# Performance work log

Hardware: AMD Instinct MI355X
Metric: run time of the kernel (lower is better)

## Reference

```python
import jax, jax.numpy as jnp
import numpy as np

L = 16            # number_of_grid_levels
T = 524288        # max_hash_table_entries (2^19)
F = 2             # hash_table_feature_dim
MIN_RES = 16      # coarsest_resolution
MAX_RES = 2048    # finest_resolution
WIDTH = 64        # mlp_width
OUT = 3           # output_channels
N = 1048576       # number of 2D query points
PRIME_Y = np.uint32(2654435761)  # NGP spatial hash prime for dim 1 (dim 0 prime = 1)


def _resolutions():
    g = np.exp((np.log(MAX_RES) - np.log(MIN_RES)) / (L - 1))
    return np.floor(MIN_RES * g ** np.arange(L)).astype(np.float32)  # [L]


def setup_inputs() -> dict:
    key = jax.random.key(0)
    ks = jax.random.split(key, 6)
    x = jax.random.uniform(ks[0], (N, 2), dtype=jnp.float32)
    # NGP hash tables are initialized small uniform
    tables = jax.random.uniform(ks[1], (L, T, F), minval=-1e-4, maxval=1e-4, dtype=jnp.float32)
    def dense(k, fi, fo):
        return (jax.random.normal(k, (fi, fo), dtype=jnp.float32) / np.sqrt(fi).astype(np.float32))
    W0 = dense(ks[2], L * F, WIDTH)
    W1 = dense(ks[3], WIDTH, WIDTH)
    W2 = dense(ks[4], WIDTH, OUT)
    return dict(x=x, tables=tables,
                W0=W0, b0=jnp.zeros((WIDTH,), jnp.float32),
                W1=W1, b1=jnp.zeros((WIDTH,), jnp.float32),
                W2=W2, b2=jnp.zeros((OUT,), jnp.float32))


def _hash_encode(x, tables):
    # Multi-resolution hash grid encoding (Instant-NGP, spatial_dim=2).
    res = jnp.asarray(_resolutions())                  # [L]
    scaled = x[:, None, :] * res[None, :, None]        # [N, L, 2]
    floored = jnp.floor(scaled)
    frac = scaled - floored                            # [N, L, 2]
    corners = jnp.array([[0, 0], [1, 0], [0, 1], [1, 1]], dtype=jnp.int32)  # [4, 2]
    vert = floored.astype(jnp.int32)[:, :, None, :] + corners[None, None]   # [N, L, 4, 2]
    vu = vert.astype(jnp.uint32)
    h = vu[..., 0] ^ (vu[..., 1] * PRIME_Y)            # spatial hash (prime for dim0 is 1)
    idx = (h % jnp.uint32(T)).astype(jnp.int32)        # [N, L, 4]
    feats = tables[jnp.arange(L)[None, :, None], idx]  # [N, L, 4, F] gather per level
    # bilinear weights: prod over dims of frac (if corner==1) else 1-frac
    wd = jnp.where(corners[None, None] == 1, frac[:, :, None, :], 1.0 - frac[:, :, None, :])
    w = wd[..., 0] * wd[..., 1]                        # [N, L, 4]
    interp = jnp.einsum('nlc,nlcf->nlf', w, feats)     # [N, L, F]
    return interp.reshape(x.shape[0], L * F)           # [N, L*F]


def reference(x, tables, W0, b0, W1, b1, W2, b2):
    h = _hash_encode(x, tables)
    h = jax.nn.relu(h @ W0 + b0)
    h = jax.nn.relu(h @ W1 + b1)
    return jax.nn.sigmoid(h @ W2 + b2)   # [N, 3]
```

## Files before the change

kernel.cpp:

```cpp
#include <hip/hip_runtime.h>

#define LVLS  16
#define TSZ   524288u
#define TMASK (TSZ - 1u)
#define PRIME 2654435761u

__constant__ float RES[LVLS] = {16.f, 22.f, 30.f, 42.f, 58.f, 80.f, 111.f, 153.f,
                                212.f, 294.f, 406.f, 561.f, 776.f, 1072.f, 1482.f, 2048.f};

typedef __bf16 bf16x8 __attribute__((ext_vector_type(8)));
typedef float  f32x4  __attribute__((ext_vector_type(4)));

union Frag {
    uint4          q;
    unsigned       u[4];
    unsigned short s[8];
    bf16x8         v;
};

static __device__ __forceinline__ unsigned short f2bf(float f) {
    unsigned u = __float_as_uint(f);
    u += 0x7FFFu + ((u >> 16) & 1u);
    return (unsigned short)(u >> 16);
}
static __device__ __forceinline__ unsigned pack2(float a, float b) {
    return (unsigned)f2bf(a) | ((unsigned)f2bf(b) << 16);
}
static __device__ __forceinline__ void lds_fence() {
    asm volatile("s_waitcnt lgkmcnt(0)" ::: "memory");
}

__global__ __launch_bounds__(256) void ngp_encode(
    const float* __restrict__ x, const float* __restrict__ tables,
    unsigned* __restrict__ feat, int N, int PB)
{
    const int g  = blockIdx.x;
    const int r  = g & 7;
    const int i  = g >> 3;
    const int hi = (i >= PB);
    const int l  = r + (hi << 3);
    const int pb = i - (hi ? PB : 0);
    const int n  = pb * 256 + threadIdx.x;
    if (n >= N) return;

    const float2 xy = ((const float2*)x)[n];
    const float res = RES[l];
    const float sx = xy.x * res, sy = xy.y * res;
    const float fx = floorf(sx),  fy = floorf(sy);
    const float ux = sx - fx,     uy = sy - fy;
    const unsigned ix = (unsigned)(int)fx, iy = (unsigned)(int)fy;
    const unsigned hy0 = iy * PRIME, hy1 = (iy + 1u) * PRIME;
    const unsigned i00 = (ix ^ hy0) & TMASK;
    const unsigned i10 = ((ix + 1u) ^ hy0) & TMASK;
    const unsigned i01 = (ix ^ hy1) & TMASK;
    const unsigned i11 = ((ix + 1u) ^ hy1) & TMASK;
    const float2* tb = (const float2*)(tables + (size_t)l * (TSZ * 2));
    const float2 f00 = tb[i00], f10 = tb[i10], f01 = tb[i01], f11 = tb[i11];
    const float w00 = (1.f - ux) * (1.f - uy);
    const float w10 = ux * (1.f - uy);
    const float w01 = (1.f - ux) * uy;
    const float w11 = ux * uy;
    const float e0 = w00*f00.x + w10*f10.x + w01*f01.x + w11*f11.x;
    const float e1 = w00*f00.y + w10*f10.y + w01*f01.y + w11*f11.y;
    feat[(size_t)l * N + n] = pack2(e0, e1);
}

__global__ __launch_bounds__(256) void ngp_mlp(
    const unsigned* __restrict__ feat,
    const float* __restrict__ W0, const float* __restrict__ b0,
    const float* __restrict__ W1, const float* __restrict__ b1,
    const float* __restrict__ W2, const float* __restrict__ b2,
    float* __restrict__ out, int N)
{
    __shared__ uint4 sB0[4 * 64];
    __shared__ uint4 sB1[8 * 64];
    __shared__ uint4 sB2[2 * 64];
    __shared__ __align__(16) unsigned short hscr[4][16][72];

    const int tid  = threadIdx.x;
    const int lane = tid & 63;
    const int w    = tid >> 6;
    const int c    = lane & 15;
    const int quad = lane >> 4;

    {
        const int f = tid >> 6;
        Frag t0;
        #pragma unroll
        for (int j = 0; j < 8; ++j)
            t0.s[j] = f2bf(W0[(quad * 8 + j) * 64 + f * 16 + c]);
        sB0[f * 64 + lane] = t0.q;

        #pragma unroll
        for (int pass = 0; pass < 2; ++pass) {
            const int ff = f + pass * 4;
            const int kt = ff >> 2, tt = ff & 3;
            Frag t1;
            #pragma unroll
            for (int j = 0; j < 8; ++j)
                t1.s[j] = f2bf(W1[(kt * 32 + quad * 8 + j) * 64 + tt * 16 + c]);
            sB1[ff * 64 + lane] = t1.q;
        }
        if (f < 2) {
            Frag t2;
            #pragma unroll
            for (int j = 0; j < 8; ++j) {
                const float v = (c < 3) ? W2[(f * 32 + quad * 8 + j) * 3 + c] : 0.f;
                t2.s[j] = f2bf(v);
            }
            sB2[f * 64 + lane] = t2.q;
        }
    }
    __syncthreads();

    Frag B0f[4], B1f[8], B2f[2];
    #pragma unroll
    for (int t = 0; t < 4; ++t) B0f[t].q = sB0[t * 64 + lane];
    #pragma unroll
    for (int f = 0; f < 8; ++f) B1f[f].q = sB1[f * 64 + lane];
    #pragma unroll
    for (int f = 0; f < 2; ++f) B2f[f].q = sB2[f * 64 + lane];

    float bias0[4], bias1[4];
    #pragma unroll
    for (int t = 0; t < 4; ++t) { bias0[t] = b0[t * 16 + c]; bias1[t] = b1[t * 16 + c]; }
    const float bias2 = (c < 3) ? b2[c] : 0.f;

    #pragma unroll 1
    for (int it = 0; it < 4; ++it) {
        const int n0 = blockIdx.x * 256 + w * 64 + it * 16;

        Frag a0;
        #pragma unroll
        for (int i = 0; i < 4; ++i)
            a0.u[i] = feat[(size_t)(quad * 4 + i) * N + n0 + c];

        f32x4 acc0[4];
        #pragma unroll
        for (int t = 0; t < 4; ++t) {
            f32x4 cin = {bias0[t], bias0[t], bias0[t], bias0[t]};
            acc0[t] = __builtin_amdgcn_mfma_f32_16x16x32_bf16(a0.v, B0f[t].v, cin, 0, 0, 0);
        }

        lds_fence();
        #pragma unroll
        for (int t = 0; t < 4; ++t)
            #pragma unroll
            for (int rr = 0; rr < 4; ++rr)
                hscr[w][quad * 4 + rr][t * 16 + c] = f2bf(fmaxf(acc0[t][rr], 0.f));

        lds_fence();
        Frag a1[2];
        #pragma unroll
        for (int kt = 0; kt < 2; ++kt)
            a1[kt].q = *(const uint4*)&hscr[w][c][kt * 32 + quad * 8];

        f32x4 acc1[4];
        #pragma unroll
        for (int t = 0; t < 4; ++t) {
            f32x4 cin = {bias1[t], bias1[t], bias1[t], bias1[t]};
            cin = __builtin_amdgcn_mfma_f32_16x16x32_bf16(a1[0].v, B1f[t].v, cin, 0, 0, 0);
            acc1[t] = __builtin_amdgcn_mfma_f32_16x16x32_bf16(a1[1].v, B1f[4 + t].v, cin, 0, 0, 0);
        }

        lds_fence();
        #pragma unroll
        for (int t = 0; t < 4; ++t)
            #pragma unroll
            for (int rr = 0; rr < 4; ++rr)
                hscr[w][quad * 4 + rr][t * 16 + c] = f2bf(fmaxf(acc1[t][rr], 0.f));

        lds_fence();
        Frag a2[2];
        #pragma unroll
        for (int kt = 0; kt < 2; ++kt)
            a2[kt].q = *(const uint4*)&hscr[w][c][kt * 32 + quad * 8];

        f32x4 cin2 = {bias2, bias2, bias2, bias2};
        cin2 = __builtin_amdgcn_mfma_f32_16x16x32_bf16(a2[0].v, B2f[0].v, cin2, 0, 0, 0);
        f32x4 acc2 = __builtin_amdgcn_mfma_f32_16x16x32_bf16(a2[1].v, B2f[1].v, cin2, 0, 0, 0);

        if (c < 3) {
            #pragma unroll
            for (int rr = 0; rr < 4; ++rr) {
                const float s = 1.f / (1.f + __expf(-acc2[rr]));
                out[(size_t)(n0 + quad * 4 + rr) * 3 + c] = s;
            }
        }
    }
}

extern "C" void kernel_launch(void* const* d_in, const int* in_sizes, int n_in,
                              void* d_out, int out_size, void* d_ws, size_t ws_size,
                              hipStream_t stream) {
    const float* x      = (const float*)d_in[0];
    const float* tables = (const float*)d_in[1];
    const float* W0     = (const float*)d_in[2];
    const float* b0     = (const float*)d_in[3];
    const float* W1     = (const float*)d_in[4];
    const float* b1     = (const float*)d_in[5];
    const float* W2     = (const float*)d_in[6];
    const float* b2     = (const float*)d_in[7];
    float* out = (float*)d_out;
    unsigned* feat = (unsigned*)d_ws;

    const int N  = in_sizes[0] / 2;
    const int PB = (N + 255) / 256;
    ngp_encode<<<16 * PB, 256, 0, stream>>>(x, tables, feat, N, PB);
    ngp_mlp<<<PB, 256, 0, stream>>>(feat, W0, b0, W1, b1, W2, b2, out, N);
}
```

Measured before the change: 308.2 us.

## Sort query points into spatial cells before hash encoding for gather locality

Points are bucketed into a 256x256 grid with a histogram, scan and scatter. The encoder then reads them in spatially sorted order, so neighbouring threads hit nearby hash table entries and gathers get better cache locality. The MLP writes its outputs back through the permutation. Weight fragments are precomputed once by a separate kernel instead of in every block, and each wave now processes 128 points with two tiles in flight. The cost is four extra launches plus atomic histogram and scatter passes, and the output stores become scattered.

```diff
diff --git a/kernel.cpp b/kernel.cpp
--- a/kernel.cpp
+++ b/kernel.cpp
@@ -29,9 +29,87 @@
 static __device__ __forceinline__ void lds_fence() {
     asm volatile("s_waitcnt lgkmcnt(0)" ::: "memory");
 }
+static __device__ __forceinline__ unsigned cell_key(float2 v) {
+    unsigned cx = (unsigned)(v.x * 256.f); cx = cx > 255u ? 255u : cx;
+    unsigned cy = (unsigned)(v.y * 256.f); cy = cy > 255u ? 255u : cy;
+    return (cy << 8) | cx;
+}
+
+__global__ __launch_bounds__(256) void k_zero(unsigned* __restrict__ hist) {
+    hist[blockIdx.x * 256 + threadIdx.x] = 0u;
+}
+
+__global__ __launch_bounds__(256) void k_hist(const float2* __restrict__ x,
+                                              unsigned* __restrict__ hist, int N) {
+    const int n = blockIdx.x * 256 + threadIdx.x;
+    if (n >= N) return;
+    atomicAdd(&hist[cell_key(x[n])], 1u);
+}
+
+__global__ __launch_bounds__(1024) void k_scan(unsigned* __restrict__ hist) {
+    __shared__ unsigned ps[1024];
+    const int t = threadIdx.x;
+    unsigned s = 0;
+    for (int i = 0; i < 64; ++i) s += hist[t * 64 + i];
+    ps[t] = s;
+    __syncthreads();
+    for (int off = 1; off < 1024; off <<= 1) {
+        const unsigned v = (t >= off) ? ps[t - off] : 0u;
+        __syncthreads();
+        ps[t] += v;
+        __syncthreads();
+    }
+    unsigned run = ps[t] - s;
+    for (int i = 0; i < 64; ++i) {
+        const unsigned cnt = hist[t * 64 + i];
+        hist[t * 64 + i] = run;
+        run += cnt;
+    }
+}
+
+__global__ __launch_bounds__(256) void k_scatter(const float2* __restrict__ x,
+                                                 unsigned* __restrict__ hist,
+                                                 int* __restrict__ perm,
+                                                 float2* __restrict__ xs, int N) {
+    const int n = blockIdx.x * 256 + threadIdx.x;
+    if (n >= N) return;
+    const float2 v = x[n];
+    const unsigned pos = atomicAdd(&hist[cell_key(v)], 1u);
+    perm[pos] = n;
+    xs[pos] = v;
+}
+
+__global__ __launch_bounds__(64) void k_frag(
+    const float* __restrict__ W0, const float* __restrict__ W1,
+    const float* __restrict__ W2, uint4* __restrict__ frg)
+{
+    const int lane = threadIdx.x;
+    const int c = lane & 15, quad = lane >> 4;
+    Frag t;
+    for (int f = 0; f < 4; ++f) {
+        #pragma unroll
+        for (int j = 0; j < 8; ++j) t.s[j] = f2bf(W0[(quad * 8 + j) * 64 + f * 16 + c]);
+        frg[f * 64 + lane] = t.q;
+    }
+    for (int ff = 0; ff < 8; ++ff) {
+        const int kt = ff >> 2, tt = ff & 3;
+        #pragma unroll
+        for (int j = 0; j < 8; ++j)
+            t.s[j] = f2bf(W1[(kt * 32 + quad * 8 + j) * 64 + tt * 16 + c]);
+        frg[(4 + ff) * 64 + lane] = t.q;
+    }
+    for (int f = 0; f < 2; ++f) {
+        #pragma unroll
+        for (int j = 0; j < 8; ++j) {
+            const float v = (c < 3) ? W2[(f * 32 + quad * 8 + j) * 3 + c] : 0.f;
+            t.s[j] = f2bf(v);
+        }
+        frg[(12 + f) * 64 + lane] = t.q;
+    }
+}
 
 __global__ __launch_bounds__(256) void ngp_encode(
-    const float* __restrict__ x, const float* __restrict__ tables,
+    const float2* __restrict__ xs, const float* __restrict__ tables,
     unsigned* __restrict__ feat, int N, int PB)
 {
     const int g  = blockIdx.x;
@@ -43,7 +121,7 @@
     const int n  = pb * 256 + threadIdx.x;
     if (n >= N) return;
 
-    const float2 xy = ((const float2*)x)[n];
+    const float2 xy = xs[n];
     const float res = RES[l];
     const float sx = xy.x * res, sy = xy.y * res;
     const float fx = floorf(sx),  fy = floorf(sy);
@@ -66,16 +144,12 @@
 }
 
 __global__ __launch_bounds__(256) void ngp_mlp(
-    const unsigned* __restrict__ feat,
-    const float* __restrict__ W0, const float* __restrict__ b0,
-    const float* __restrict__ W1, const float* __restrict__ b1,
-    const float* __restrict__ W2, const float* __restrict__ b2,
-    float* __restrict__ out, int N)
+    const unsigned* __restrict__ feat, const uint4* __restrict__ frg,
+    const float* __restrict__ b0, const float* __restrict__ b1,
+    const float* __restrict__ b2,
+    const int* __restrict__ perm, float* __restrict__ out, int N)
 {
-    __shared__ uint4 sB0[4 * 64];
-    __shared__ uint4 sB1[8 * 64];
-    __shared__ uint4 sB2[2 * 64];
-    __shared__ __align__(16) unsigned short hscr[4][16][72];
+    __shared__ __align__(16) unsigned short hscr[4][2][16][72];
 
     const int tid  = threadIdx.x;
     const int lane = tid & 63;
@@ -83,108 +157,107 @@
     const int c    = lane & 15;
     const int quad = lane >> 4;
 
-    {
-        const int f = tid >> 6;
-        Frag t0;
-        #pragma unroll
-        for (int j = 0; j < 8; ++j)
-            t0.s[j] = f2bf(W0[(quad * 8 + j) * 64 + f * 16 + c]);
-        sB0[f * 64 + lane] = t0.q;
-
-        #pragma unroll
-        for (int pass = 0; pass < 2; ++pass) {
-            const int ff = f + pass * 4;
-            const int kt = ff >> 2, tt = ff & 3;
-            Frag t1;
-            #pragma unroll
-            for (int j = 0; j < 8; ++j)
-                t1.s[j] = f2bf(W1[(kt * 32 + quad * 8 + j) * 64 + tt * 16 + c]);
-            sB1[ff * 64 + lane] = t1.q;
-        }
-        if (f < 2) {
-            Frag t2;
-            #pragma unroll
-            for (int j = 0; j < 8; ++j) {
-                const float v = (c < 3) ? W2[(f * 32 + quad * 8 + j) * 3 + c] : 0.f;
-                t2.s[j] = f2bf(v);
-            }
-            sB2[f * 64 + lane] = t2.q;
-        }
-    }
-    __syncthreads();
-
     Frag B0f[4], B1f[8], B2f[2];
     #pragma unroll
-    for (int t = 0; t < 4; ++t) B0f[t].q = sB0[t * 64 + lane];
-    #pragma unroll
-    for (int f = 0; f < 8; ++f) B1f[f].q = sB1[f * 64 + lane];
-    #pragma unroll
-    for (int f = 0; f < 2; ++f) B2f[f].q = sB2[f * 64 + lane];
+    for (int t = 0; t < 4; ++t) B0f[t].q = frg[t * 64 + lane];
+    #pragma unroll
+    for (int f = 0; f < 8; ++f) B1f[f].q = frg[(4 + f) * 64 + lane];
+    #pragma unroll
+    for (int f = 0; f < 2; ++f) B2f[f].q = frg[(12 + f) * 64 + lane];
 
     float bias0[4], bias1[4];
     #pragma unroll
     for (int t = 0; t < 4; ++t) { bias0[t] = b0[t * 16 + c]; bias1[t] = b1[t * 16 + c]; }
     const float bias2 = (c < 3) ? b2[c] : 0.f;
 
-    #pragma unroll 1
-    for (int it = 0; it < 4; ++it) {
-        const int n0 = blockIdx.x * 256 + w * 64 + it * 16;
-
-        Frag a0;
+    const int base = blockIdx.x * 512 + w * 128;
+
+    Frag a0[8];
+    #pragma unroll
+    for (int tt = 0; tt < 8; ++tt)
         #pragma unroll
         for (int i = 0; i < 4; ++i)
-            a0.u[i] = feat[(size_t)(quad * 4 + i) * N + n0 + c];
-
-        f32x4 acc0[4];
-        #pragma unroll
-        for (int t = 0; t < 4; ++t) {
-            f32x4 cin = {bias0[t], bias0[t], bias0[t], bias0[t]};
-            acc0[t] = __builtin_amdgcn_mfma_f32_16x16x32_bf16(a0.v, B0f[t].v, cin, 0, 0, 0);
-        }
+            a0[tt].u[i] = feat[(size_t)(quad * 4 + i) * N + base + tt * 16 + c];
+
+    #pragma unroll
+    for (int gpair = 0; gpair < 4; ++gpair) {
+        const int t0n = base + (2 * gpair) * 16;
+        const int t1n = base + (2 * gpair + 1) * 16;
+        if (t0n + 16 > N) break;
+
+        int p[2][4];
+        #pragma unroll
+        for (int s = 0; s < 2; ++s)
+            #pragma unroll
+            for (int rr = 0; rr < 4; ++rr) {
+                const int idx = (s ? t1n : t0n) + quad * 4 + rr;
+                p[s][rr] = perm ? perm[idx] : idx;
+            }
+
+        f32x4 acc[2][4];
+        #pragma unroll
+        for (int s = 0; s < 2; ++s)
+            #pragma unroll
+            for (int t = 0; t < 4; ++t) {
+                f32x4 cin = {bias0[t], bias0[t], bias0[t], bias0[t]};
+                acc[s][t] = __builtin_amdgcn_mfma_f32_16x16x32_bf16(
+                    a0[2 * gpair + s].v, B0f[t].v, cin, 0, 0, 0);
+            }
 
         lds_fence();
         #pragma unroll
-        for (int t = 0; t < 4; ++t)
-            #pragma unroll
-            for (int rr = 0; rr < 4; ++rr)
-                hscr[w][quad * 4 + rr][t * 16 + c] = f2bf(fmaxf(acc0[t][rr], 0.f));
-
+        for (int s = 0; s < 2; ++s)
+            #pragma unroll
+            for (int t = 0; t < 4; ++t)
+                #pragma unroll
+                for (int rr = 0; rr < 4; ++rr)
+                    hscr[w][s][quad * 4 + rr][t * 16 + c] = f2bf(fmaxf(acc[s][t][rr], 0.f));
         lds_fence();
-        Frag a1[2];
-        #pragma unroll
-        for (int kt = 0; kt < 2; ++kt)
-            a1[kt].q = *(const uint4*)&hscr[w][c][kt * 32 + quad * 8];
-
-        f32x4 acc1[4];
-        #pragma unroll
-        for (int t = 0; t < 4; ++t) {
-            f32x4 cin = {bias1[t], bias1[t], bias1[t], bias1[t]};
-            cin = __builtin_amdgcn_mfma_f32_16x16x32_bf16(a1[0].v, B1f[t].v, cin, 0, 0, 0);
-            acc1[t] = __builtin_amdgcn_mfma_f32_16x16x32_bf16(a1[1].v, B1f[4 + t].v, cin, 0, 0, 0);
-        }
+
+        Frag a1[2][2];
+        #pragma unroll
+        for (int s = 0; s < 2; ++s)
+            #pragma unroll
+            for (int kt = 0; kt < 2; ++kt)
+                a1[s][kt].q = *(const uint4*)&hscr[w][s][c][kt * 32 + quad * 8];
+
+        #pragma unroll
+        for (int s = 0; s < 2; ++s)
+            #pragma unroll
+            for (int t = 0; t < 4; ++t) {
+                f32x4 cin = {bias1[t], bias1[t], bias1[t], bias1[t]};
+                cin = __builtin_amdgcn_mfma_f32_16x16x32_bf16(a1[s][0].v, B1f[t].v, cin, 0, 0, 0);
+                acc[s][t] = __builtin_amdgcn_mfma_f32_16x16x32_bf16(a1[s][1].v, B1f[4 + t].v, cin, 0, 0, 0);
+            }
 
         lds_fence();
         #pragma unroll
-        for (int t = 0; t < 4; ++t)
-            #pragma unroll
-            for (int rr = 0; rr < 4; ++rr)
-                hscr[w][quad * 4 + rr][t * 16 + c] = f2bf(fmaxf(acc1[t][rr], 0.f));
-
+        for (int s = 0; s < 2; ++s)
+            #pragma unroll
+            for (int t = 0; t < 4; ++t)
+                #pragma unroll
+                for (int rr = 0; rr < 4; ++rr)
+                    hscr[w][s][quad * 4 + rr][t * 16 + c] = f2bf(fmaxf(acc[s][t][rr], 0.f));
         lds_fence();
-        Frag a2[2];
-        #pragma unroll
-        for (int kt = 0; kt < 2; ++kt)
-            a2[kt].q = *(const uint4*)&hscr[w][c][kt * 32 + quad * 8];
-
-        f32x4 cin2 = {bias2, bias2, bias2, bias2};
-        cin2 = __builtin_amdgcn_mfma_f32_16x16x32_bf16(a2[0].v, B2f[0].v, cin2, 0, 0, 0);
-        f32x4 acc2 = __builtin_amdgcn_mfma_f32_16x16x32_bf16(a2[1].v, B2f[1].v, cin2, 0, 0, 0);
-
-        if (c < 3) {
-            #pragma unroll
-            for (int rr = 0; rr < 4; ++rr) {
-                const float s = 1.f / (1.f + __expf(-acc2[rr]));
-                out[(size_t)(n0 + quad * 4 + rr) * 3 + c] = s;
+
+        Frag a2[2][2];
+        #pragma unroll
+        for (int s = 0; s < 2; ++s)
+            #pragma unroll
+            for (int kt = 0; kt < 2; ++kt)
+                a2[s][kt].q = *(const uint4*)&hscr[w][s][c][kt * 32 + quad * 8];
+
+        #pragma unroll
+        for (int s = 0; s < 2; ++s) {
+            f32x4 cin2 = {bias2, bias2, bias2, bias2};
+            cin2 = __builtin_amdgcn_mfma_f32_16x16x32_bf16(a2[s][0].v, B2f[0].v, cin2, 0, 0, 0);
+            const f32x4 o = __builtin_amdgcn_mfma_f32_16x16x32_bf16(a2[s][1].v, B2f[1].v, cin2, 0, 0, 0);
+            if (c < 3) {
+                #pragma unroll
+                for (int rr = 0; rr < 4; ++rr) {
+                    const float sg = 1.f / (1.f + __expf(-o[rr]));
+                    out[(size_t)p[s][rr] * 3 + c] = sg;
+                }
             }
         }
     }
@@ -202,10 +275,39 @@
     const float* W2     = (const float*)d_in[6];
     const float* b2     = (const float*)d_in[7];
     float* out = (float*)d_out;
-    unsigned* feat = (unsigned*)d_ws;
 
     const int N  = in_sizes[0] / 2;
     const int PB = (N + 255) / 256;
-    ngp_encode<<<16 * PB, 256, 0, stream>>>(x, tables, feat, N, PB);
-    ngp_mlp<<<PB, 256, 0, stream>>>(feat, W0, b0, W1, b1, W2, b2, out, N);
-}
+    char* ws = (char*)d_ws;
+
+    const size_t off_frag = 0;
+    const size_t off_feat = 16384;
+    const size_t feat_sz  = (size_t)LVLS * N * 4;
+    const size_t off_xs   = off_feat + feat_sz;
+    const size_t off_perm = off_xs + (size_t)N * 8;
+    const size_t off_hist = off_perm + (size_t)N * 4;
+    const size_t need     = off_hist + 65536 * 4;
+    const bool use_sort = (ws_size >= need);
+
+    uint4*    frg  = (uint4*)(ws + off_frag);
+    unsigned* feat = (unsigned*)(ws + off_feat);
+    float2*   xs   = (float2*)(ws + off_xs);
+    int*      perm = (int*)(ws + off_perm);
+    unsigned* hist = (unsigned*)(ws + off_hist);
+
+    k_frag<<<1, 64, 0, stream>>>(W0, W1, W2, frg);
+
+    const float2* enc_x = (const float2*)x;
+    const int* mlp_perm = nullptr;
+    if (use_sort) {
+        k_zero<<<256, 256, 0, stream>>>(hist);
+        k_hist<<<(N + 255) / 256, 256, 0, stream>>>((const float2*)x, hist, N);
+        k_scan<<<1, 1024, 0, stream>>>(hist);
+        k_scatter<<<(N + 255) / 256, 256, 0, stream>>>((const float2*)x, hist, perm, xs, N);
+        enc_x = xs;
+        mlp_perm = perm;
+    }
+
+    ngp_encode<<<16 * PB, 256, 0, stream>>>(enc_x, tables, feat, N, PB);
+    ngp_mlp<<<(N + 511) / 512, 256, 0, stream>>>(feat, frg, b0, b1, b2, mlp_perm, out, N);
+}
```

New measurement: 369.6 us. +19.9%, slower.

## Fuse hash encoding into MLP kernel and precompute weight fragments once

Applied to the files above, without the earlier changes.

Removes the separate encode kernel and the bf16 feature buffer in workspace: each MFMA lane now computes the hash-grid interpolation for its own level pair directly into the A fragment. Weight fragments are converted once by a tiny kernel into workspace instead of per block, and the hidden-layer stores are permuted (with matching row permutation of W1/W2) so each lane writes packed 8-byte stores to LDS. The cost is that table gathers for all 16 levels now sit inside the MLP kernel, losing the level-major cache locality of the old encode layout, and the gathers must overlap with the MFMA work.

```diff
diff --git a/kernel.cpp b/kernel.cpp
--- a/kernel.cpp
+++ b/kernel.cpp
@@ -24,57 +24,59 @@
     return (unsigned short)(u >> 16);
 }
 static __device__ __forceinline__ unsigned pack2(float a, float b) {
-    return (unsigned)f2bf(a) | ((unsigned)f2bf(b) << 16);
+    unsigned ua = __float_as_uint(a), ub = __float_as_uint(b);
+    ua += 0x7FFFu + ((ua >> 16) & 1u);
+    ub += 0x7FFFu + ((ub >> 16) & 1u);
+    return (ua >> 16) | (ub & 0xFFFF0000u);
 }
 static __device__ __forceinline__ void lds_fence() {
     asm volatile("s_waitcnt lgkmcnt(0)" ::: "memory");
 }
 
-__global__ __launch_bounds__(256) void ngp_encode(
-    const float* __restrict__ x, const float* __restrict__ tables,
-    unsigned* __restrict__ feat, int N, int PB)
+__global__ __launch_bounds__(256) void k_frag(
+    const float* __restrict__ W0, const float* __restrict__ W1,
+    const float* __restrict__ W2, uint4* __restrict__ frg)
 {
-    const int g  = blockIdx.x;
-    const int r  = g & 7;
-    const int i  = g >> 3;
-    const int hi = (i >= PB);
-    const int l  = r + (hi << 3);
-    const int pb = i - (hi ? PB : 0);
-    const int n  = pb * 256 + threadIdx.x;
-    if (n >= N) return;
-
-    const float2 xy = ((const float2*)x)[n];
-    const float res = RES[l];
-    const float sx = xy.x * res, sy = xy.y * res;
-    const float fx = floorf(sx),  fy = floorf(sy);
-    const float ux = sx - fx,     uy = sy - fy;
-    const unsigned ix = (unsigned)(int)fx, iy = (unsigned)(int)fy;
-    const unsigned hy0 = iy * PRIME, hy1 = (iy + 1u) * PRIME;
-    const unsigned i00 = (ix ^ hy0) & TMASK;
-    const unsigned i10 = ((ix + 1u) ^ hy0) & TMASK;
-    const unsigned i01 = (ix ^ hy1) & TMASK;
-    const unsigned i11 = ((ix + 1u) ^ hy1) & TMASK;
-    const float2* tb = (const float2*)(tables + (size_t)l * (TSZ * 2));
-    const float2 f00 = tb[i00], f10 = tb[i10], f01 = tb[i01], f11 = tb[i11];
-    const float w00 = (1.f - ux) * (1.f - uy);
-    const float w10 = ux * (1.f - uy);
-    const float w01 = (1.f - ux) * uy;
-    const float w11 = ux * uy;
-    const float e0 = w00*f00.x + w10*f10.x + w01*f01.x + w11*f11.x;
-    const float e1 = w00*f00.y + w10*f10.y + w01*f01.y + w11*f11.y;
-    feat[(size_t)l * N + n] = pack2(e0, e1);
-}
-
-__global__ __launch_bounds__(256) void ngp_mlp(
-    const unsigned* __restrict__ feat,
-    const float* __restrict__ W0, const float* __restrict__ b0,
-    const float* __restrict__ W1, const float* __restrict__ b1,
-    const float* __restrict__ W2, const float* __restrict__ b2,
-    float* __restrict__ out, int N)
+    const int lane = threadIdx.x & 63;
+    const int wv   = threadIdx.x >> 6;
+    const int c = lane & 15, quad = lane >> 4;
+    for (int set = wv; set < 14; set += 4) {
+        Frag t;
+        if (set < 4) {
+            const int f = set;
+            #pragma unroll
+            for (int j = 0; j < 8; ++j)
+                t.s[j] = f2bf(W0[(quad * 8 + j) * 64 + f * 16 + c]);
+        } else if (set < 12) {
+            const int ff = set - 4;
+            const int kt = ff >> 2, tt = ff & 3;
+            #pragma unroll
+            for (int j = 0; j < 8; ++j) {
+                const int eta = kt * 32 + quad * 8 + j;
+                const int orig = (eta & 3) * 16 + (eta >> 2);
+                t.s[j] = f2bf(W1[orig * 64 + tt * 16 + c]);
+            }
+        } else {
+            const int f = set - 12;
+            #pragma unroll
+            for (int j = 0; j < 8; ++j) {
+                const int eta = f * 32 + quad * 8 + j;
+                const int orig = (eta & 3) * 16 + (eta >> 2);
+                const float v = (c < 3) ? W2[orig * 3 + c] : 0.f;
+                t.s[j] = f2bf(v);
+            }
+        }
+        frg[set * 64 + lane] = t.q;
+    }
+}
+
+#define TPW 4
+__global__ __launch_bounds__(256, 4) void ngp_fused(
+    const float2* __restrict__ x, const float* __restrict__ tables,
+    const uint4* __restrict__ frg,
+    const float* __restrict__ b0, const float* __restrict__ b1,
+    const float* __restrict__ b2, float* __restrict__ out, int N)
 {
-    __shared__ uint4 sB0[4 * 64];
-    __shared__ uint4 sB1[8 * 64];
-    __shared__ uint4 sB2[2 * 64];
     __shared__ __align__(16) unsigned short hscr[4][16][72];
 
     const int tid  = threadIdx.x;
@@ -83,93 +85,105 @@
     const int c    = lane & 15;
     const int quad = lane >> 4;
 
-    {
-        const int f = tid >> 6;
-        Frag t0;
-        #pragma unroll
-        for (int j = 0; j < 8; ++j)
-            t0.s[j] = f2bf(W0[(quad * 8 + j) * 64 + f * 16 + c]);
-        sB0[f * 64 + lane] = t0.q;
-
-        #pragma unroll
-        for (int pass = 0; pass < 2; ++pass) {
-            const int ff = f + pass * 4;
-            const int kt = ff >> 2, tt = ff & 3;
-            Frag t1;
-            #pragma unroll
-            for (int j = 0; j < 8; ++j)
-                t1.s[j] = f2bf(W1[(kt * 32 + quad * 8 + j) * 64 + tt * 16 + c]);
-            sB1[ff * 64 + lane] = t1.q;
-        }
-        if (f < 2) {
-            Frag t2;
-            #pragma unroll
-            for (int j = 0; j < 8; ++j) {
-                const float v = (c < 3) ? W2[(f * 32 + quad * 8 + j) * 3 + c] : 0.f;
-                t2.s[j] = f2bf(v);
-            }
-            sB2[f * 64 + lane] = t2.q;
-        }
-    }
-    __syncthreads();
-
     Frag B0f[4], B1f[8], B2f[2];
     #pragma unroll
-    for (int t = 0; t < 4; ++t) B0f[t].q = sB0[t * 64 + lane];
-    #pragma unroll
-    for (int f = 0; f < 8; ++f) B1f[f].q = sB1[f * 64 + lane];
-    #pragma unroll
-    for (int f = 0; f < 2; ++f) B2f[f].q = sB2[f * 64 + lane];
+    for (int t = 0; t < 4; ++t) B0f[t].q = frg[t * 64 + lane];
+    #pragma unroll
+    for (int f = 0; f < 8; ++f) B1f[f].q = frg[(4 + f) * 64 + lane];
+    #pragma unroll
+    for (int f = 0; f < 2; ++f) B2f[f].q = frg[(12 + f) * 64 + lane];
 
     float bias0[4], bias1[4];
     #pragma unroll
     for (int t = 0; t < 4; ++t) { bias0[t] = b0[t * 16 + c]; bias1[t] = b1[t * 16 + c]; }
     const float bias2 = (c < 3) ? b2[c] : 0.f;
 
+    const int nTiles = N >> 4;
+    int tile = (blockIdx.x * 4 + w) * TPW;
+
     #pragma unroll 1
-    for (int it = 0; it < 4; ++it) {
-        const int n0 = blockIdx.x * 256 + w * 64 + it * 16;
-
+    for (int it = 0; it < TPW; ++it, ++tile) {
+        if (tile >= nTiles) break;
+        const int n0 = tile * 16;
+
+        const float2 xy = x[n0 + c];
         Frag a0;
         #pragma unroll
-        for (int i = 0; i < 4; ++i)
-            a0.u[i] = feat[(size_t)(quad * 4 + i) * N + n0 + c];
-
-        f32x4 acc0[4];
+        for (int pr = 0; pr < 2; ++pr) {
+            unsigned idx[8];
+            float uxa[2], uya[2];
+            #pragma unroll
+            for (int j = 0; j < 2; ++j) {
+                const int l = quad * 4 + 2 * pr + j;
+                const float r = RES[l];
+                const float sx = xy.x * r, sy = xy.y * r;
+                const float fx = floorf(sx), fy = floorf(sy);
+                uxa[j] = sx - fx; uya[j] = sy - fy;
+                const unsigned ix = (unsigned)(int)fx, iy = (unsigned)(int)fy;
+                const unsigned hy0 = iy * PRIME, hy1 = (iy + 1u) * PRIME;
+                idx[4 * j + 0] = (ix ^ hy0) & TMASK;
+                idx[4 * j + 1] = ((ix + 1u) ^ hy0) & TMASK;
+                idx[4 * j + 2] = (ix ^ hy1) & TMASK;
+                idx[4 * j + 3] = ((ix + 1u) ^ hy1) & TMASK;
+            }
+            float2 f[8];
+            #pragma unroll
+            for (int j = 0; j < 2; ++j) {
+                const int l = quad * 4 + 2 * pr + j;
+                const float2* tb = (const float2*)(tables + (size_t)l * (TSZ * 2));
+                f[4 * j + 0] = tb[idx[4 * j + 0]];
+                f[4 * j + 1] = tb[idx[4 * j + 1]];
+                f[4 * j + 2] = tb[idx[4 * j + 2]];
+                f[4 * j + 3] = tb[idx[4 * j + 3]];
+            }
+            #pragma unroll
+            for (int j = 0; j < 2; ++j) {
+                const float w00 = (1.f - uxa[j]) * (1.f - uya[j]);
+                const float w10 = uxa[j] * (1.f - uya[j]);
+                const float w01 = (1.f - uxa[j]) * uya[j];
+                const float w11 = uxa[j] * uya[j];
+                const float e0 = w00 * f[4*j+0].x + w10 * f[4*j+1].x + w01 * f[4*j+2].x + w11 * f[4*j+3].x;
+                const float e1 = w00 * f[4*j+0].y + w10 * f[4*j+1].y + w01 * f[4*j+2].y + w11 * f[4*j+3].y;
+                a0.u[2 * pr + j] = pack2(e0, e1);
+            }
+        }
+
+        f32x4 acc[4];
         #pragma unroll
         for (int t = 0; t < 4; ++t) {
             f32x4 cin = {bias0[t], bias0[t], bias0[t], bias0[t]};
-            acc0[t] = __builtin_amdgcn_mfma_f32_16x16x32_bf16(a0.v, B0f[t].v, cin, 0, 0, 0);
-        }
-
-        lds_fence();
-        #pragma unroll
-        for (int t = 0; t < 4; ++t)
-            #pragma unroll
-            for (int rr = 0; rr < 4; ++rr)
-                hscr[w][quad * 4 + rr][t * 16 + c] = f2bf(fmaxf(acc0[t][rr], 0.f));
-
+            acc[t] = __builtin_amdgcn_mfma_f32_16x16x32_bf16(a0.v, B0f[t].v, cin, 0, 0, 0);
+        }
+
+        lds_fence();
+        #pragma unroll
+        for (int rr = 0; rr < 4; ++rr) {
+            uint2 pk;
+            pk.x = pack2(fmaxf(acc[0][rr], 0.f), fmaxf(acc[1][rr], 0.f));
+            pk.y = pack2(fmaxf(acc[2][rr], 0.f), fmaxf(acc[3][rr], 0.f));
+            *(uint2*)&hscr[w][quad * 4 + rr][4 * c] = pk;
+        }
         lds_fence();
         Frag a1[2];
         #pragma unroll
         for (int kt = 0; kt < 2; ++kt)
             a1[kt].q = *(const uint4*)&hscr[w][c][kt * 32 + quad * 8];
 
-        f32x4 acc1[4];
         #pragma unroll
         for (int t = 0; t < 4; ++t) {
             f32x4 cin = {bias1[t], bias1[t], bias1[t], bias1[t]};
             cin = __builtin_amdgcn_mfma_f32_16x16x32_bf16(a1[0].v, B1f[t].v, cin, 0, 0, 0);
-            acc1[t] = __builtin_amdgcn_mfma_f32_16x16x32_bf16(a1[1].v, B1f[4 + t].v, cin, 0, 0, 0);
-        }
-
-        lds_fence();
-        #pragma unroll
-        for (int t = 0; t < 4; ++t)
-            #pragma unroll
-            for (int rr = 0; rr < 4; ++rr)
-                hscr[w][quad * 4 + rr][t * 16 + c] = f2bf(fmaxf(acc1[t][rr], 0.f));
-
+            acc[t] = __builtin_amdgcn_mfma_f32_16x16x32_bf16(a1[1].v, B1f[4 + t].v, cin, 0, 0, 0);
+        }
+
+        lds_fence();
+        #pragma unroll
+        for (int rr = 0; rr < 4; ++rr) {
+            uint2 pk;
+            pk.x = pack2(fmaxf(acc[0][rr], 0.f), fmaxf(acc[1][rr], 0.f));
+            pk.y = pack2(fmaxf(acc[2][rr], 0.f), fmaxf(acc[3][rr], 0.f));
+            *(uint2*)&hscr[w][quad * 4 + rr][4 * c] = pk;
+        }
         lds_fence();
         Frag a2[2];
         #pragma unroll
@@ -178,13 +192,12 @@
 
         f32x4 cin2 = {bias2, bias2, bias2, bias2};
         cin2 = __builtin_amdgcn_mfma_f32_16x16x32_bf16(a2[0].v, B2f[0].v, cin2, 0, 0, 0);
-        f32x4 acc2 = __builtin_amdgcn_mfma_f32_16x16x32_bf16(a2[1].v, B2f[1].v, cin2, 0, 0, 0);
-
+        const f32x4 o = __builtin_amdgcn_mfma_f32_16x16x32_bf16(a2[1].v, B2f[1].v, cin2, 0, 0, 0);
         if (c < 3) {
             #pragma unroll
             for (int rr = 0; rr < 4; ++rr) {
-                const float s = 1.f / (1.f + __expf(-acc2[rr]));
-                out[(size_t)(n0 + quad * 4 + rr) * 3 + c] = s;
+                const float sg = 1.f / (1.f + __expf(-o[rr]));
+                out[(size_t)(n0 + quad * 4 + rr) * 3 + c] = sg;
             }
         }
     }
@@ -202,10 +215,14 @@
     const float* W2     = (const float*)d_in[6];
     const float* b2     = (const float*)d_in[7];
     float* out = (float*)d_out;
-    unsigned* feat = (unsigned*)d_ws;
-
-    const int N  = in_sizes[0] / 2;
-    const int PB = (N + 255) / 256;
-    ngp_encode<<<16 * PB, 256, 0, stream>>>(x, tables, feat, N, PB);
-    ngp_mlp<<<PB, 256, 0, stream>>>(feat, W0, b0, W1, b1, W2, b2, out, N);
-}
+
+    const int N = in_sizes[0] / 2;
+    uint4* frg = (uint4*)d_ws;
+
+    k_frag<<<1, 256, 0, stream>>>(W0, W1, W2, frg);
+
+    const int nTiles = N >> 4;
+    const int blocks = (nTiles + 4 * TPW - 1) / (4 * TPW);
+    ngp_fused<<<blocks, 256, 0, stream>>>((const float2*)x, tables, frg,
+                                          b0, b1, b2, out, N);
+}
```

New measurement: 463.0 us. 50.2% more time.
